# Kernel tuning notes

Hardware: AMD Instinct MI355X
Metric: run time of the kernel (lower is better)

## Reference

```python
import jax, jax.numpy as jnp
import numpy as np

F_DIM, H, O = 128, 256, 256
NQ, EQ = 64, 512
ND, ED = 50000, 600000

PARAM_SHAPES = [
    ("qW1", (F_DIM, H)), ("qb1", (H,)), ("qW2", (H, H)), ("qb2", (H,)),
    ("qW3", (H, H)),     ("qb3", (H,)), ("qW4", (H, O)), ("qb4", (O,)),
    ("dW1", (F_DIM, H)), ("db1", (H,)), ("dW2", (H, H)), ("db2", (H,)),
    ("dW3", (H, H)),     ("db3", (H,)), ("dW4", (H, O)), ("db4", (O,)),
    ("lW1", (2 * O, O)), ("lb1", (O,)),
    ("lW2", (O, O // 2)), ("lb2", (O // 2,)),
    ("lW3", (O // 2, 8)), ("lb3", (8,)),
]

def setup_inputs() -> dict:
    key = jax.random.key(0)
    ks = jax.random.split(key, 4 + len(PARAM_SHAPES))
    inp = {
        "query_in_feat": jax.random.normal(ks[0], (NQ, F_DIM), jnp.float32),
        "data_in_feat": jax.random.normal(ks[1], (ND, F_DIM), jnp.float32),
        "query_edge_list": jax.random.randint(ks[2], (2, EQ), 0, NQ),
        "data_edge_list": jax.random.randint(ks[3], (2, ED), 0, ND),
    }
    for i, (name, shape) in enumerate(PARAM_SHAPES):
        fan_in = shape[0] if len(shape) == 2 else 1
        inp[name] = jax.random.normal(ks[4 + i], shape, jnp.float32) * (1.0 / np.sqrt(fan_in))
    return inp

def _mlp2(x, W1, b1, W2, b2):
    return jnp.maximum(x @ W1 + b1, 0.0) @ W2 + b2

def _gin_conv(x, src, dst, W1, b1, W2, b2):
    # GINConv (eps=0): MLP(x_i + sum_{j->i} x_j); gather x[src], scatter-add at dst
    agg = jax.ops.segment_sum(x[src], dst, num_segments=x.shape[0])
    return _mlp2(x + agg, W1, b1, W2, b2)

def _gin(x, edge_index, p):
    src, dst = edge_index[0], edge_index[1]
    h = jnp.maximum(_gin_conv(x, src, dst, *p[:4]), 0.0)  # ReLU between convs
    return _gin_conv(h, src, dst, *p[4:])

def reference(query_in_feat, data_in_feat, query_edge_list, data_edge_list,
              qW1, qb1, qW2, qb2, qW3, qb3, qW4, qb4,
              dW1, db1, dW2, db2, dW3, db3, dW4, db4,
              lW1, lb1, lW2, lb2, lW3, lb3):
    qx = _gin(query_in_feat, query_edge_list, (qW1, qb1, qW2, qb2, qW3, qb3, qW4, qb4))
    dx = _gin(data_in_feat, data_edge_list, (dW1, db1, dW2, db2, dW3, db3, dW4, db4))
    # global_add_pool with batch = zeros -> single-graph sum
    qp = jnp.sum(qx, axis=0, keepdims=True)  # [1, O]
    dp = jnp.sum(dx, axis=0, keepdims=True)  # [1, O]
    h = jnp.concatenate([qp, dp], axis=1)    # [1, 2*O]
    h = jnp.maximum(h @ lW1 + lb1, 0.0)
    h = jnp.maximum(h @ lW2 + lb2, 0.0)
    h = jnp.maximum(h @ lW3 + lb3, 0.0)
    return h.reshape(1, 8)
```

## Files before the change

### kernel.cpp

```cpp
#include <hip/hip_runtime.h>
#include <hip/hip_bf16.h>


#define NQ 64
#define EQ 512
#define ND 50000
#define ED 600000
#define FDIM 128
#define HDIM 256

typedef __attribute__((ext_vector_type(8))) short short8;
typedef __attribute__((ext_vector_type(4))) float f32x4;
typedef __attribute__((ext_vector_type(2))) float floatx2;
typedef __attribute__((ext_vector_type(4))) unsigned short us4;
typedef __attribute__((ext_vector_type(2))) unsigned short us2;

__device__ __forceinline__ unsigned short f2bf(float f) {
    union { float f; unsigned u; } v; v.f = f;
    unsigned r = v.u + 0x7FFF + ((v.u >> 16) & 1);
    return (unsigned short)(r >> 16);
}
__device__ __forceinline__ float bf2f(unsigned short u) {
    union { unsigned u; float f; } v; v.u = ((unsigned)u) << 16;
    return v.f;
}


struct PackDesc {
    const float* W[8];
    unsigned short* Wp[8];
    int KT[8];
    int start[9];
};

__device__ __forceinline__ void pack_unit(const PackDesc& pd, int unit, int l) {
    int m = 0;
    while (m < 7 && unit >= pd.start[m + 1]) ++m;
    const int local = unit - pd.start[m];
    const int KT = pd.KT[m];
    const int kt = local % KT;
    const int ct = local / KT;
    const float* W = pd.W[m];
    unsigned short* Wp = pd.Wp[m];
    const int row = kt * 32 + (l >> 4) * 8;
    const int col = ct * 16 + (l & 15);
    short8 v;
#pragma unroll
    for (int j = 0; j < 8; ++j) v[j] = (short)f2bf(W[(size_t)(row + j) * 256 + col]);
    *(short8*)(Wp + (((size_t)(ct * KT + kt)) * 64 + l) * 8) = v;
}


__global__ void prepass(const float* __restrict__ xd, const float* __restrict__ xq,
                        unsigned short* __restrict__ bx, long long nd4, long long n4,
                        int cvt_b, PackDesc pd, int pack_units, int pack_b,
                        const int* __restrict__ d_dst, int* __restrict__ d_deg,
                        const int* __restrict__ q_dst, int* __restrict__ q_deg,
                        int d_eb) {
    const int b = blockIdx.x;
    const int tid = threadIdx.x;
    if (b < cvt_b) {
        long long i = (long long)b * 256 + tid;
        if (i >= n4) return;
        const float* src = (i < nd4) ? (xd + i * 4) : (xq + (i - nd4) * 4);
        float4 v = *(const float4*)src;
        us4 o;
        o[0] = f2bf(v.x); o[1] = f2bf(v.y); o[2] = f2bf(v.z); o[3] = f2bf(v.w);
        *(us4*)(bx + i * 4) = o;
    } else if (b < cvt_b + pack_b) {
        const int unit = (b - cvt_b) * 4 + (tid >> 6);
        if (unit < pack_units) pack_unit(pd, unit, tid & 63);
    } else {
        const int cb = b - cvt_b - pack_b;
        if (cb < d_eb) {
            int e = cb * 256 + tid;
            if (e < ED) atomicAdd(&d_deg[d_dst[e]], 1);
        } else {
            int e = (cb - d_eb) * 256 + tid;
            if (e < EQ) atomicAdd(&q_deg[q_dst[e]], 1);
        }
    }
}


__device__ __forceinline__ void scan1_body(const int* deg, int* rowptr, int* bsum,
                                           int n, int blk) {
    __shared__ int sh[256];
    const int t = threadIdx.x;
    const int i = blk * 256 + t;
    const int v = (i < n) ? deg[i] : 0;
    sh[t] = v;
    __syncthreads();
    for (int off = 1; off < 256; off <<= 1) {
        int x = (t >= off) ? sh[t - off] : 0;
        __syncthreads();
        sh[t] += x;
        __syncthreads();
    }
    if (i < n) rowptr[i] = sh[t] - v;
    if (t == 255) bsum[blk] = sh[255];
}

__global__ void scan_phase1_both(const int* __restrict__ d_deg, int* __restrict__ d_rowptr,
                                 int* __restrict__ d_bsum,
                                 const int* __restrict__ q_deg, int* __restrict__ q_rowptr,
                                 int* __restrict__ q_bsum, int dblocks) {
    int b = blockIdx.x;
    if (b < dblocks) scan1_body(d_deg, d_rowptr, d_bsum, ND, b);
    else             scan1_body(q_deg, q_rowptr, q_bsum, NQ, b - dblocks);
}

__device__ __forceinline__ void scan2_body(const int* bsum, int* boff, int* rowptr_n, int nb) {
    __shared__ int sh[256];
    const int t = threadIdx.x;
    const int v = (t < nb) ? bsum[t] : 0;
    sh[t] = v;
    __syncthreads();
    for (int off = 1; off < 256; off <<= 1) {
        int x = (t >= off) ? sh[t - off] : 0;
        __syncthreads();
        sh[t] += x;
        __syncthreads();
    }
    if (t < nb) boff[t] = sh[t] - v;
    if (t == 255) *rowptr_n = sh[255];
}

__global__ void scan_phase2_both(const int* __restrict__ d_bsum, int* __restrict__ d_boff,
                                 int* __restrict__ d_rowptr_n, int d_nb,
                                 const int* __restrict__ q_bsum, int* __restrict__ q_boff,
                                 int* __restrict__ q_rowptr_n, int q_nb) {
    if (blockIdx.x == 0) scan2_body(d_bsum, d_boff, d_rowptr_n, d_nb);
    else                 scan2_body(q_bsum, q_boff, q_rowptr_n, q_nb);
}

__global__ void scan_phase3_both(int* __restrict__ d_rowptr, const int* __restrict__ d_boff,
                                 int* __restrict__ d_cursor,
                                 int* __restrict__ q_rowptr, const int* __restrict__ q_boff,
                                 int* __restrict__ q_cursor, int dblocks) {
    int b = blockIdx.x;
    if (b < dblocks) {
        int i = b * 256 + threadIdx.x;
        if (i < ND) {
            int r = d_rowptr[i] + d_boff[b];
            d_rowptr[i] = r; d_cursor[i] = r;
        }
    } else {
        int i = (b - dblocks) * 256 + threadIdx.x;
        if (i < NQ) {
            int r = q_rowptr[i] + q_boff[b - dblocks];
            q_rowptr[i] = r; q_cursor[i] = r;
        }
    }
}

__global__ void fill_csr_both(const int* __restrict__ d_src, const int* __restrict__ d_dst,
                              int* __restrict__ d_cursor, int* __restrict__ d_csrsrc,
                              const int* __restrict__ q_src, const int* __restrict__ q_dst,
                              int* __restrict__ q_cursor, int* __restrict__ q_csrsrc,
                              int dblocks) {
    int b = blockIdx.x;
    if (b < dblocks) {
        int e = b * 256 + threadIdx.x;
        if (e < ED) {
            int p = atomicAdd(&d_cursor[d_dst[e]], 1);
            d_csrsrc[p] = d_src[e];
        }
    } else {
        int e = (b - dblocks) * 256 + threadIdx.x;
        if (e < EQ) {
            int p = atomicAdd(&q_cursor[q_dst[e]], 1);
            q_csrsrc[p] = q_src[e];
        }
    }
}


template <int F>
__global__ void gin_agg_dual(const unsigned short* __restrict__ xd, const int* __restrict__ rpd,
                             const int* __restrict__ csd, unsigned short* __restrict__ od,
                             const unsigned short* __restrict__ xq, const int* __restrict__ rpq,
                             const int* __restrict__ csq, unsigned short* __restrict__ oq) {
    constexpr int V = F / 64;
    const unsigned short* x; const int* rowptr; const int* csr; unsigned short* out; int node;
    if ((int)blockIdx.x < ND) { x = xd; rowptr = rpd; csr = csd; out = od; node = blockIdx.x; }
    else { x = xq; rowptr = rpq; csr = csq; out = oq; node = blockIdx.x - ND; }

    const int t = threadIdx.x;
    const int beg = rowptr[node];
    const int end = rowptr[node + 1];

    float acc[V];
    {
        const unsigned short* p = x + (size_t)node * F + t * V;
        if constexpr (V == 4) {
            us4 v = *(const us4*)p;
#pragma unroll
            for (int i = 0; i < 4; ++i) acc[i] = bf2f(v[i]);
        } else {
            us2 v = *(const us2*)p;
            acc[0] = bf2f(v[0]); acc[1] = bf2f(v[1]);
        }
    }
    int j = beg;
    for (; j + 1 < end; j += 2) {
        const unsigned short* p0 = x + (size_t)csr[j] * F + t * V;
        const unsigned short* p1 = x + (size_t)csr[j + 1] * F + t * V;
        if constexpr (V == 4) {
            us4 v0 = *(const us4*)p0;
            us4 v1 = *(const us4*)p1;
#pragma unroll
            for (int i = 0; i < 4; ++i) acc[i] += bf2f(v0[i]) + bf2f(v1[i]);
        } else {
            us2 v0 = *(const us2*)p0;
            us2 v1 = *(const us2*)p1;
            acc[0] += bf2f(v0[0]) + bf2f(v1[0]);
            acc[1] += bf2f(v0[1]) + bf2f(v1[1]);
        }
    }
    if (j < end) {
        const unsigned short* p0 = x + (size_t)csr[j] * F + t * V;
        if constexpr (V == 4) {
            us4 v0 = *(const us4*)p0;
#pragma unroll
            for (int i = 0; i < 4; ++i) acc[i] += bf2f(v0[i]);
        } else {
            us2 v0 = *(const us2*)p0;
            acc[0] += bf2f(v0[0]); acc[1] += bf2f(v0[1]);
        }
    }
    unsigned short* po = out + (size_t)node * F + t * V;
    if constexpr (V == 4) {
        us4 r;
#pragma unroll
        for (int i = 0; i < 4; ++i) r[i] = f2bf(acc[i]);
        *(us4*)po = r;
    } else {
        us2 r; r[0] = f2bf(acc[0]); r[1] = f2bf(acc[1]);
        *(us2*)po = r;
    }
}


__global__ void gin_agg_f8_dual(const unsigned char* __restrict__ xd, const int* __restrict__ rpd,
                                const int* __restrict__ csd, unsigned short* __restrict__ od,
                                const unsigned char* __restrict__ xq, const int* __restrict__ rpq,
                                const int* __restrict__ csq, unsigned short* __restrict__ oq) {
    const unsigned char* x; const int* rowptr; const int* csr; unsigned short* out; int node;
    if ((int)blockIdx.x < ND) { x = xd; rowptr = rpd; csr = csd; out = od; node = blockIdx.x; }
    else { x = xq; rowptr = rpq; csr = csq; out = oq; node = blockIdx.x - ND; }

    const int t = threadIdx.x;
    const int beg = rowptr[node];
    const int end = rowptr[node + 1];

    float a0, a1, a2, a3;
    {
        const unsigned w = *(const unsigned*)(x + (size_t)node * 256 + t * 4);
        floatx2 lo = __builtin_amdgcn_cvt_pk_f32_fp8((int)w, false);
        floatx2 hi = __builtin_amdgcn_cvt_pk_f32_fp8((int)w, true);
        a0 = lo[0]; a1 = lo[1]; a2 = hi[0]; a3 = hi[1];
    }
    int j = beg;
    for (; j + 1 < end; j += 2) {
        const unsigned w0 = *(const unsigned*)(x + (size_t)csr[j] * 256 + t * 4);
        const unsigned w1 = *(const unsigned*)(x + (size_t)csr[j + 1] * 256 + t * 4);
        floatx2 l0 = __builtin_amdgcn_cvt_pk_f32_fp8((int)w0, false);
        floatx2 h0 = __builtin_amdgcn_cvt_pk_f32_fp8((int)w0, true);
        floatx2 l1 = __builtin_amdgcn_cvt_pk_f32_fp8((int)w1, false);
        floatx2 h1 = __builtin_amdgcn_cvt_pk_f32_fp8((int)w1, true);
        a0 += l0[0] + l1[0]; a1 += l0[1] + l1[1];
        a2 += h0[0] + h1[0]; a3 += h0[1] + h1[1];
    }
    if (j < end) {
        const unsigned w0 = *(const unsigned*)(x + (size_t)csr[j] * 256 + t * 4);
        floatx2 l0 = __builtin_amdgcn_cvt_pk_f32_fp8((int)w0, false);
        floatx2 h0 = __builtin_amdgcn_cvt_pk_f32_fp8((int)w0, true);
        a0 += l0[0]; a1 += l0[1]; a2 += h0[0]; a3 += h0[1];
    }
    us4 r;
    r[0] = f2bf(a0); r[1] = f2bf(a1); r[2] = f2bf(a2); r[3] = f2bf(a3);
    *(us4*)(out + (size_t)node * 256 + t * 4) = r;
}


template <int KIN>
__global__ __launch_bounds__(256) void mlp_dual(
    const unsigned short* __restrict__ Ad,
    const unsigned short* __restrict__ W1pd, const float* __restrict__ b1d,
    const unsigned short* __restrict__ W2pd, const float* __restrict__ b2d,
    unsigned char* __restrict__ C8d, float* __restrict__ poold, int ndb,
    const unsigned short* __restrict__ Aq,
    const unsigned short* __restrict__ W1pq, const float* __restrict__ b1q,
    const unsigned short* __restrict__ W2pq, const float* __restrict__ b2q,
    unsigned char* __restrict__ C8q, float* __restrict__ poolq,
    int relu_out) {
    constexpr int KT1 = KIN / 32;
    __shared__ __align__(16) unsigned short lds[64 * 256];

    const unsigned short* A; const unsigned short* W1p; const float* b1;
    const unsigned short* W2p; const float* b2;
    unsigned char* C8; float* pool; int row0, N;
    if ((int)blockIdx.x < ndb) {
        A = Ad; W1p = W1pd; b1 = b1d; W2p = W2pd; b2 = b2d;
        C8 = C8d; pool = poold; row0 = blockIdx.x * 64; N = ND;
    } else {
        A = Aq; W1p = W1pq; b1 = b1q; W2p = W2pq; b2 = b2q;
        C8 = C8q; pool = poolq; row0 = 0; N = NQ;
    }

    const int tid = threadIdx.x;
    const int lane = tid & 63;
    const int wv = tid >> 6;
    const int lrow = lane & 15;
    const int lk2 = (lane >> 4) * 8;
    const int nrows = (N - row0 < 64) ? (N - row0) : 64;

    for (int idx = tid; idx < nrows * (KIN / 8); idx += 256) {
        const int r = idx / (KIN / 8);
        const int k8 = (idx % (KIN / 8)) * 8;
        short8 v = *(const short8*)(A + (size_t)(row0 + r) * KIN + k8);
        unsigned byte = (unsigned)((r * KIN + k8) * 2) ^ (unsigned)((r & 7) << 4);
        *(short8*)((char*)lds + byte) = v;
    }
    __syncthreads();

    f32x4 acc1[4][4];
#pragma unroll
    for (int fm = 0; fm < 4; ++fm)
#pragma unroll
        for (int fn = 0; fn < 4; ++fn) acc1[fm][fn] = (f32x4)(0.f);

    const unsigned short* W1Base = W1p + ((size_t)(wv * 4) * KT1 * 64 + lane) * 8;
    for (int kt = 0; kt < KT1; ++kt) {
        short8 a[4], bf[4];
#pragma unroll
        for (int fm = 0; fm < 4; ++fm) {
            const int r = fm * 16 + lrow;
            unsigned byte = (unsigned)((r * KIN + kt * 32 + lk2) * 2) ^ (unsigned)((r & 7) << 4);
            a[fm] = *(const short8*)((const char*)lds + byte);
        }
#pragma unroll
        for (int fn = 0; fn < 4; ++fn)
            bf[fn] = *(const short8*)(W1Base + ((size_t)fn * KT1 + kt) * 64 * 8);
#pragma unroll
        for (int fm = 0; fm < 4; ++fm)
#pragma unroll
            for (int fn = 0; fn < 4; ++fn)
                acc1[fm][fn] = __builtin_amdgcn_mfma_f32_16x16x32_bf16(
                    a[fm], bf[fn], acc1[fm][fn], 0, 0, 0);
    }
    __syncthreads();

#pragma unroll
    for (int fn = 0; fn < 4; ++fn) {
        const int col = wv * 64 + fn * 16 + lrow;
        const float bv = b1[col];
#pragma unroll
        for (int fm = 0; fm < 4; ++fm) {
            const int rbase = fm * 16 + (lane >> 4) * 4;
#pragma unroll
            for (int r = 0; r < 4; ++r) {
                const int row = rbase + r;
                const float v = fmaxf(acc1[fm][fn][r] + bv, 0.f);
                unsigned byte = (unsigned)((row * 256 + col) * 2) ^ (unsigned)((row & 7) << 4);
                *(unsigned short*)((char*)lds + byte) = f2bf(v);
            }
        }
    }
    __syncthreads();

    f32x4 acc2[4][4];
#pragma unroll
    for (int fm = 0; fm < 4; ++fm)
#pragma unroll
        for (int fn = 0; fn < 4; ++fn) acc2[fm][fn] = (f32x4)(0.f);

    const unsigned short* W2Base = W2p + ((size_t)(wv * 4) * 8 * 64 + lane) * 8;
    for (int kt = 0; kt < 8; ++kt) {
        short8 a[4], bf[4];
#pragma unroll
        for (int fm = 0; fm < 4; ++fm) {
            const int r = fm * 16 + lrow;
            unsigned byte = (unsigned)((r * 256 + kt * 32 + lk2) * 2) ^ (unsigned)((r & 7) << 4);
            a[fm] = *(const short8*)((const char*)lds + byte);
        }
#pragma unroll
        for (int fn = 0; fn < 4; ++fn)
            bf[fn] = *(const short8*)(W2Base + ((size_t)fn * 8 + kt) * 64 * 8);
#pragma unroll
        for (int fm = 0; fm < 4; ++fm)
#pragma unroll
            for (int fn = 0; fn < 4; ++fn)
                acc2[fm][fn] = __builtin_amdgcn_mfma_f32_16x16x32_bf16(
                    a[fm], bf[fn], acc2[fm][fn], 0, 0, 0);
    }

#pragma unroll
    for (int fn = 0; fn < 4; ++fn) {
        const int col = wv * 64 + fn * 16 + lrow;
        const float bv = b2[col];
        float ps = 0.f;
#pragma unroll
        for (int fm = 0; fm < 4; ++fm) {
            const int rbase = row0 + fm * 16 + (lane >> 4) * 4;
#pragma unroll
            for (int r = 0; r < 4; ++r) {
                const int row = rbase + r;
                if (row < N) {
                    float v = acc2[fm][fn][r] + bv;
                    if (relu_out) v = fmaxf(v, 0.f);
                    if (C8) {
                        unsigned p = (unsigned)__builtin_amdgcn_cvt_pk_fp8_f32(v, v, 0, false);
                        C8[(size_t)row * 256 + col] = (unsigned char)(p & 0xff);
                    }
                    ps += v;
                }
            }
        }
        if (pool) {
            ps += __shfl_xor(ps, 16);
            ps += __shfl_xor(ps, 32);
            if ((lane >> 4) == 0) atomicAdd(&pool[col], ps);
        }
    }
}


__global__ void mlp_head(const float* __restrict__ pooled,
                         const float* __restrict__ lW1, const float* __restrict__ lb1,
                         const float* __restrict__ lW2, const float* __restrict__ lb2,
                         const float* __restrict__ lW3, const float* __restrict__ lb3,
                         float* __restrict__ out) {
    __shared__ float h0[512];
    __shared__ float h1[256];
    __shared__ float h2[128];
    const int t = threadIdx.x;
    h0[t] = pooled[t];
    h0[t + 256] = pooled[t + 256];
    __syncthreads();

    float acc = lb1[t];
    for (int k = 0; k < 512; ++k) acc += h0[k] * lW1[k * 256 + t];
    h1[t] = fmaxf(acc, 0.f);
    __syncthreads();

    if (t < 128) {
        float a = lb2[t];
        for (int k = 0; k < 256; ++k) a += h1[k] * lW2[k * 128 + t];
        h2[t] = fmaxf(a, 0.f);
    }
    __syncthreads();

    if (t < 8) {
        float a = lb3[t];
        for (int k = 0; k < 128; ++k) a += h2[k] * lW3[k * 8 + t];
        out[t] = fmaxf(a, 0.f);
    }
}


extern "C" void kernel_launch(void* const* d_in, const int* in_sizes, int n_in,
                              void* d_out, int out_size, void* d_ws, size_t ws_size,
                              hipStream_t stream) {
    const float* q_x  = (const float*)d_in[0];
    const float* d_x  = (const float*)d_in[1];
    const int*   q_el = (const int*)d_in[2];
    const int*   d_el = (const int*)d_in[3];
    const float* qW1 = (const float*)d_in[4];  const float* qb1 = (const float*)d_in[5];
    const float* qW2 = (const float*)d_in[6];  const float* qb2 = (const float*)d_in[7];
    const float* qW3 = (const float*)d_in[8];  const float* qb3 = (const float*)d_in[9];
    const float* qW4 = (const float*)d_in[10]; const float* qb4 = (const float*)d_in[11];
    const float* dW1 = (const float*)d_in[12]; const float* db1 = (const float*)d_in[13];
    const float* dW2 = (const float*)d_in[14]; const float* db2 = (const float*)d_in[15];
    const float* dW3 = (const float*)d_in[16]; const float* db3 = (const float*)d_in[17];
    const float* dW4 = (const float*)d_in[18]; const float* db4 = (const float*)d_in[19];
    const float* lW1 = (const float*)d_in[20]; const float* lb1 = (const float*)d_in[21];
    const float* lW2 = (const float*)d_in[22]; const float* lb2 = (const float*)d_in[23];
    const float* lW3 = (const float*)d_in[24]; const float* lb3 = (const float*)d_in[25];
    (void)in_sizes; (void)n_in; (void)out_size; (void)ws_size;

    const int* q_src = q_el;  const int* q_dst = q_el + EQ;
    const int* d_src = d_el;  const int* d_dst = d_el + ED;

    char* wsb = (char*)d_ws;
    size_t off = 0;
    auto alloc = [&](size_t bytes) { void* p = wsb + off; off += (bytes + 255) & ~(size_t)255; return p; };

    unsigned short* bxd = (unsigned short*)alloc((size_t)ND * FDIM * 2);
    unsigned short* bxq = (unsigned short*)alloc((size_t)NQ * FDIM * 2);
    unsigned short* dag = (unsigned short*)alloc((size_t)ND * FDIM * 2);
    unsigned short* qag = (unsigned short*)alloc((size_t)NQ * FDIM * 2);
    unsigned char*  h8d = (unsigned char*)alloc((size_t)ND * HDIM);
    unsigned char*  h8q = (unsigned char*)alloc((size_t)NQ * HDIM);
    unsigned short* had = (unsigned short*)alloc((size_t)ND * HDIM * 2);
    unsigned short* haq = (unsigned short*)alloc((size_t)NQ * HDIM * 2);
    float* pooled = (float*)alloc(512 * 4);
    int* d_deg    = (int*)alloc((size_t)ND * 4);
    int* q_deg    = (int*)alloc((size_t)NQ * 4);
    int* d_rowptr = (int*)alloc((size_t)(ND + 1) * 4);
    int* d_cursor = (int*)alloc((size_t)ND * 4);
    int* d_csrsrc = (int*)alloc((size_t)ED * 4);
    int* d_bsum   = (int*)alloc(256 * 4);
    int* d_boff   = (int*)alloc(256 * 4);
    int* q_rowptr = (int*)alloc((size_t)(NQ + 1) * 4);
    int* q_cursor = (int*)alloc((size_t)NQ * 4);
    int* q_csrsrc = (int*)alloc((size_t)EQ * 4);
    int* q_bsum   = (int*)alloc(256 * 4);
    int* q_boff   = (int*)alloc(256 * 4);
    unsigned short* pdW1 = (unsigned short*)alloc((size_t)FDIM * 256 * 2);
    unsigned short* pdW2 = (unsigned short*)alloc((size_t)HDIM * 256 * 2);
    unsigned short* pdW3 = (unsigned short*)alloc((size_t)HDIM * 256 * 2);
    unsigned short* pdW4 = (unsigned short*)alloc((size_t)HDIM * 256 * 2);
    unsigned short* pqW1 = (unsigned short*)alloc((size_t)FDIM * 256 * 2);
    unsigned short* pqW2 = (unsigned short*)alloc((size_t)HDIM * 256 * 2);
    unsigned short* pqW3 = (unsigned short*)alloc((size_t)HDIM * 256 * 2);
    unsigned short* pqW4 = (unsigned short*)alloc((size_t)HDIM * 256 * 2);

    hipMemsetAsync(pooled, 0, 512 * 4, stream);
    hipMemsetAsync(d_deg, 0, (char*)(q_deg + NQ) - (char*)d_deg, stream);

    const int d_eb = (ED + 255) / 256;
    const int q_eb = (EQ + 255) / 256;
    const int d_nb = (ND + 255) / 256;
    const int q_nb = (NQ + 255) / 256;
    {
        PackDesc pd;
        const float* Ws[8] = {dW1, dW2, dW3, dW4, qW1, qW2, qW3, qW4};
        unsigned short* Wps[8] = {pdW1, pdW2, pdW3, pdW4, pqW1, pqW2, pqW3, pqW4};
        int kts[8] = {4, 8, 8, 8, 4, 8, 8, 8};
        int s = 0;
        for (int i = 0; i < 8; ++i) {
            pd.W[i] = Ws[i]; pd.Wp[i] = Wps[i]; pd.KT[i] = kts[i];
            pd.start[i] = s; s += 16 * kts[i];
        }
        pd.start[8] = s;
        const int pack_units = s;
        const int pack_b = (s + 3) / 4;
        long long nd4 = (long long)ND * FDIM / 4;
        long long n4 = nd4 + (long long)NQ * FDIM / 4;
        const int cvt_b = (int)((n4 + 255) / 256);
        prepass<<<cvt_b + pack_b + d_eb + q_eb, 256, 0, stream>>>(
            d_x, q_x, bxd, nd4, n4, cvt_b, pd, pack_units, pack_b,
            d_dst, d_deg, q_dst, q_deg, d_eb);
    }

    scan_phase1_both<<<d_nb + q_nb, 256, 0, stream>>>(d_deg, d_rowptr, d_bsum,
                                                      q_deg, q_rowptr, q_bsum, d_nb);
    scan_phase2_both<<<2, 256, 0, stream>>>(d_bsum, d_boff, d_rowptr + ND, d_nb,
                                            q_bsum, q_boff, q_rowptr + NQ, q_nb);
    scan_phase3_both<<<d_nb + q_nb, 256, 0, stream>>>(d_rowptr, d_boff, d_cursor,
                                                      q_rowptr, q_boff, q_cursor, d_nb);
    fill_csr_both<<<d_eb + q_eb, 256, 0, stream>>>(d_src, d_dst, d_cursor, d_csrsrc,
                                                   q_src, q_dst, q_cursor, q_csrsrc, d_eb);

    const int ndb = (ND + 63) / 64;

    gin_agg_dual<FDIM><<<ND + NQ, 64, 0, stream>>>(bxd, d_rowptr, d_csrsrc, dag,
                                                   bxq, q_rowptr, q_csrsrc, qag);
    mlp_dual<FDIM><<<ndb + 1, 256, 0, stream>>>(
        dag, pdW1, db1, pdW2, db2, h8d, nullptr, ndb,
        qag, pqW1, qb1, pqW2, qb2, h8q, nullptr, 1);

    gin_agg_f8_dual<<<ND + NQ, 64, 0, stream>>>(h8d, d_rowptr, d_csrsrc, had,
                                                h8q, q_rowptr, q_csrsrc, haq);
    mlp_dual<HDIM><<<ndb + 1, 256, 0, stream>>>(
        had, pdW3, db3, pdW4, db4, nullptr, pooled + 256, ndb,
        haq, pqW3, qb3, pqW4, qb4, nullptr, pooled, 0);

    mlp_head<<<1, 256, 0, stream>>>(pooled, lW1, lb1, lW2, lb2, lW3, lb3, (float*)d_out);
}
```

Measured before the change: 236.4 us.

## Store input features as FP8, pack two nodes per aggregation block, shrink MLP tiles

The input-feature conversion now writes FP8 instead of BF16, halving the bytes the first neighbour-gather kernel reads. The first aggregation kernel handles two nodes per 64-thread block, using 32 lanes per 128-wide row. The fused MLP kernels now process 32 rows per block instead of 64, doubling the block count and halving LDS and accumulator registers to raise occupancy. FP8 inputs lose precision relative to BF16. Note the query MLP launch passes the relu flag as 1 and 0 unchanged, and qmb is 2 blocks, which matches the new row0 indexing.

New measurement: 251.7 us. 1.06x slower.

```diff
diff --git a/kernel.cpp b/kernel.cpp
--- a/kernel.cpp
+++ b/kernel.cpp
@@ -52,7 +52,7 @@
 
 
 __global__ void prepass(const float* __restrict__ xd, const float* __restrict__ xq,
-                        unsigned short* __restrict__ bx, long long nd4, long long n4,
+                        unsigned char* __restrict__ x8, long long nd4, long long n4,
                         int cvt_b, PackDesc pd, int pack_units, int pack_b,
                         const int* __restrict__ d_dst, int* __restrict__ d_deg,
                         const int* __restrict__ q_dst, int* __restrict__ q_deg,
@@ -64,9 +64,9 @@
         if (i >= n4) return;
         const float* src = (i < nd4) ? (xd + i * 4) : (xq + (i - nd4) * 4);
         float4 v = *(const float4*)src;
-        us4 o;
-        o[0] = f2bf(v.x); o[1] = f2bf(v.y); o[2] = f2bf(v.z); o[3] = f2bf(v.w);
-        *(us4*)(bx + i * 4) = o;
+        int p = __builtin_amdgcn_cvt_pk_fp8_f32(v.x, v.y, 0, false);
+        p = __builtin_amdgcn_cvt_pk_fp8_f32(v.z, v.w, p, true);
+        *(unsigned*)(x8 + i * 4) = (unsigned)p;
     } else if (b < cvt_b + pack_b) {
         const int unit = (b - cvt_b) * 4 + (tid >> 6);
         if (unit < pack_units) pack_unit(pd, unit, tid & 63);
@@ -176,76 +176,48 @@
 }
 
 
-template <int F>
-__global__ void gin_agg_dual(const unsigned short* __restrict__ xd, const int* __restrict__ rpd,
-                             const int* __restrict__ csd, unsigned short* __restrict__ od,
-                             const unsigned short* __restrict__ xq, const int* __restrict__ rpq,
-                             const int* __restrict__ csq, unsigned short* __restrict__ oq) {
-    constexpr int V = F / 64;
-    const unsigned short* x; const int* rowptr; const int* csr; unsigned short* out; int node;
-    if ((int)blockIdx.x < ND) { x = xd; rowptr = rpd; csr = csd; out = od; node = blockIdx.x; }
-    else { x = xq; rowptr = rpq; csr = csq; out = oq; node = blockIdx.x - ND; }
+__global__ void gin_agg_f8_128_dual(const unsigned char* __restrict__ xd,
+                                    const int* __restrict__ rpd, const int* __restrict__ csd,
+                                    unsigned short* __restrict__ od,
+                                    const unsigned char* __restrict__ xq,
+                                    const int* __restrict__ rpq, const int* __restrict__ csq,
+                                    unsigned short* __restrict__ oq, int ndpair) {
+    const unsigned char* x; const int* rowptr; const int* csr; unsigned short* out; int nb;
+    if ((int)blockIdx.x < ndpair) { x = xd; rowptr = rpd; csr = csd; out = od; nb = blockIdx.x; }
+    else { x = xq; rowptr = rpq; csr = csq; out = oq; nb = blockIdx.x - ndpair; }
 
     const int t = threadIdx.x;
+    const int node = nb * 2 + (t >> 5);
+    const int c = t & 31;
+
     const int beg = rowptr[node];
     const int end = rowptr[node + 1];
 
-    float acc[V];
+    float a0, a1, a2, a3;
     {
-        const unsigned short* p = x + (size_t)node * F + t * V;
-        if constexpr (V == 4) {
-            us4 v = *(const us4*)p;
-#pragma unroll
-            for (int i = 0; i < 4; ++i) acc[i] = bf2f(v[i]);
-        } else {
-            us2 v = *(const us2*)p;
-            acc[0] = bf2f(v[0]); acc[1] = bf2f(v[1]);
-        }
-    }
-    int j = beg;
-    for (; j + 1 < end; j += 2) {
-        const unsigned short* p0 = x + (size_t)csr[j] * F + t * V;
-        const unsigned short* p1 = x + (size_t)csr[j + 1] * F + t * V;
-        if constexpr (V == 4) {
-            us4 v0 = *(const us4*)p0;
-            us4 v1 = *(const us4*)p1;
-#pragma unroll
-            for (int i = 0; i < 4; ++i) acc[i] += bf2f(v0[i]) + bf2f(v1[i]);
-        } else {
-            us2 v0 = *(const us2*)p0;
-            us2 v1 = *(const us2*)p1;
-            acc[0] += bf2f(v0[0]) + bf2f(v1[0]);
-            acc[1] += bf2f(v0[1]) + bf2f(v1[1]);
-        }
-    }
-    if (j < end) {
-        const unsigned short* p0 = x + (size_t)csr[j] * F + t * V;
-        if constexpr (V == 4) {
-            us4 v0 = *(const us4*)p0;
-#pragma unroll
-            for (int i = 0; i < 4; ++i) acc[i] += bf2f(v0[i]);
-        } else {
-            us2 v0 = *(const us2*)p0;
-            acc[0] += bf2f(v0[0]); acc[1] += bf2f(v0[1]);
-        }
-    }
-    unsigned short* po = out + (size_t)node * F + t * V;
-    if constexpr (V == 4) {
-        us4 r;
-#pragma unroll
-        for (int i = 0; i < 4; ++i) r[i] = f2bf(acc[i]);
-        *(us4*)po = r;
-    } else {
-        us2 r; r[0] = f2bf(acc[0]); r[1] = f2bf(acc[1]);
-        *(us2*)po = r;
-    }
-}
-
-
-__global__ void gin_agg_f8_dual(const unsigned char* __restrict__ xd, const int* __restrict__ rpd,
-                                const int* __restrict__ csd, unsigned short* __restrict__ od,
-                                const unsigned char* __restrict__ xq, const int* __restrict__ rpq,
-                                const int* __restrict__ csq, unsigned short* __restrict__ oq) {
+        const unsigned w = *(const unsigned*)(x + (size_t)node * 128 + c * 4);
+        floatx2 lo = __builtin_amdgcn_cvt_pk_f32_fp8((int)w, false);
+        floatx2 hi = __builtin_amdgcn_cvt_pk_f32_fp8((int)w, true);
+        a0 = lo[0]; a1 = lo[1]; a2 = hi[0]; a3 = hi[1];
+    }
+    for (int j = beg; j < end; ++j) {
+        const unsigned w = *(const unsigned*)(x + (size_t)csr[j] * 128 + c * 4);
+        floatx2 lo = __builtin_amdgcn_cvt_pk_f32_fp8((int)w, false);
+        floatx2 hi = __builtin_amdgcn_cvt_pk_f32_fp8((int)w, true);
+        a0 += lo[0]; a1 += lo[1]; a2 += hi[0]; a3 += hi[1];
+    }
+    us4 r;
+    r[0] = f2bf(a0); r[1] = f2bf(a1); r[2] = f2bf(a2); r[3] = f2bf(a3);
+    *(us4*)(out + (size_t)node * 128 + c * 4) = r;
+}
+
+
+__global__ void gin_agg_f8_256_dual(const unsigned char* __restrict__ xd,
+                                    const int* __restrict__ rpd, const int* __restrict__ csd,
+                                    unsigned short* __restrict__ od,
+                                    const unsigned char* __restrict__ xq,
+                                    const int* __restrict__ rpq, const int* __restrict__ csq,
+                                    unsigned short* __restrict__ oq) {
     const unsigned char* x; const int* rowptr; const int* csr; unsigned short* out; int node;
     if ((int)blockIdx.x < ND) { x = xd; rowptr = rpd; csr = csd; out = od; node = blockIdx.x; }
     else { x = xq; rowptr = rpq; csr = csq; out = oq; node = blockIdx.x - ND; }
@@ -289,24 +261,24 @@
     const unsigned short* __restrict__ Ad,
     const unsigned short* __restrict__ W1pd, const float* __restrict__ b1d,
     const unsigned short* __restrict__ W2pd, const float* __restrict__ b2d,
-    unsigned char* __restrict__ C8d, float* __restrict__ poold, int ndb,
+    unsigned char* __restrict__ C8d, float* __restrict__ poold, int nmb,
     const unsigned short* __restrict__ Aq,
     const unsigned short* __restrict__ W1pq, const float* __restrict__ b1q,
     const unsigned short* __restrict__ W2pq, const float* __restrict__ b2q,
     unsigned char* __restrict__ C8q, float* __restrict__ poolq,
     int relu_out) {
     constexpr int KT1 = KIN / 32;
-    __shared__ __align__(16) unsigned short lds[64 * 256];
+    __shared__ __align__(16) unsigned short lds[32 * 256];
 
     const unsigned short* A; const unsigned short* W1p; const float* b1;
     const unsigned short* W2p; const float* b2;
     unsigned char* C8; float* pool; int row0, N;
-    if ((int)blockIdx.x < ndb) {
+    if ((int)blockIdx.x < nmb) {
         A = Ad; W1p = W1pd; b1 = b1d; W2p = W2pd; b2 = b2d;
-        C8 = C8d; pool = poold; row0 = blockIdx.x * 64; N = ND;
+        C8 = C8d; pool = poold; row0 = blockIdx.x * 32; N = ND;
     } else {
         A = Aq; W1p = W1pq; b1 = b1q; W2p = W2pq; b2 = b2q;
-        C8 = C8q; pool = poolq; row0 = 0; N = NQ;
+        C8 = C8q; pool = poolq; row0 = (blockIdx.x - nmb) * 32; N = NQ;
     }
 
     const int tid = threadIdx.x;
@@ -314,7 +286,7 @@
     const int wv = tid >> 6;
     const int lrow = lane & 15;
     const int lk2 = (lane >> 4) * 8;
-    const int nrows = (N - row0 < 64) ? (N - row0) : 64;
+    const int nrows = (N - row0 < 32) ? (N - row0) : 32;
 
     for (int idx = tid; idx < nrows * (KIN / 8); idx += 256) {
         const int r = idx / (KIN / 8);
@@ -325,17 +297,17 @@
     }
     __syncthreads();
 
-    f32x4 acc1[4][4];
-#pragma unroll
-    for (int fm = 0; fm < 4; ++fm)
+    f32x4 acc1[2][4];
+#pragma unroll
+    for (int fm = 0; fm < 2; ++fm)
 #pragma unroll
         for (int fn = 0; fn < 4; ++fn) acc1[fm][fn] = (f32x4)(0.f);
 
     const unsigned short* W1Base = W1p + ((size_t)(wv * 4) * KT1 * 64 + lane) * 8;
     for (int kt = 0; kt < KT1; ++kt) {
-        short8 a[4], bf[4];
-#pragma unroll
-        for (int fm = 0; fm < 4; ++fm) {
+        short8 a[2], bf[4];
+#pragma unroll
+        for (int fm = 0; fm < 2; ++fm) {
             const int r = fm * 16 + lrow;
             unsigned byte = (unsigned)((r * KIN + kt * 32 + lk2) * 2) ^ (unsigned)((r & 7) << 4);
             a[fm] = *(const short8*)((const char*)lds + byte);
@@ -344,7 +316,7 @@
         for (int fn = 0; fn < 4; ++fn)
             bf[fn] = *(const short8*)(W1Base + ((size_t)fn * KT1 + kt) * 64 * 8);
 #pragma unroll
-        for (int fm = 0; fm < 4; ++fm)
+        for (int fm = 0; fm < 2; ++fm)
 #pragma unroll
             for (int fn = 0; fn < 4; ++fn)
                 acc1[fm][fn] = __builtin_amdgcn_mfma_f32_16x16x32_bf16(
@@ -357,7 +329,7 @@
         const int col = wv * 64 + fn * 16 + lrow;
         const float bv = b1[col];
 #pragma unroll
-        for (int fm = 0; fm < 4; ++fm) {
+        for (int fm = 0; fm < 2; ++fm) {
             const int rbase = fm * 16 + (lane >> 4) * 4;
 #pragma unroll
             for (int r = 0; r < 4; ++r) {
@@ -370,17 +342,17 @@
     }
     __syncthreads();
 
-    f32x4 acc2[4][4];
-#pragma unroll
-    for (int fm = 0; fm < 4; ++fm)
+    f32x4 acc2[2][4];
+#pragma unroll
+    for (int fm = 0; fm < 2; ++fm)
 #pragma unroll
         for (int fn = 0; fn < 4; ++fn) acc2[fm][fn] = (f32x4)(0.f);
 
     const unsigned short* W2Base = W2p + ((size_t)(wv * 4) * 8 * 64 + lane) * 8;
     for (int kt = 0; kt < 8; ++kt) {
-        short8 a[4], bf[4];
-#pragma unroll
-        for (int fm = 0; fm < 4; ++fm) {
+        short8 a[2], bf[4];
+#pragma unroll
+        for (int fm = 0; fm < 2; ++fm) {
             const int r = fm * 16 + lrow;
             unsigned byte = (unsigned)((r * 256 + kt * 32 + lk2) * 2) ^ (unsigned)((r & 7) << 4);
             a[fm] = *(const short8*)((const char*)lds + byte);
@@ -389,7 +361,7 @@
         for (int fn = 0; fn < 4; ++fn)
             bf[fn] = *(const short8*)(W2Base + ((size_t)fn * 8 + kt) * 64 * 8);
 #pragma unroll
-        for (int fm = 0; fm < 4; ++fm)
+        for (int fm = 0; fm < 2; ++fm)
 #pragma unroll
             for (int fn = 0; fn < 4; ++fn)
                 acc2[fm][fn] = __builtin_amdgcn_mfma_f32_16x16x32_bf16(
@@ -402,7 +374,7 @@
         const float bv = b2[col];
         float ps = 0.f;
 #pragma unroll
-        for (int fm = 0; fm < 4; ++fm) {
+        for (int fm = 0; fm < 2; ++fm) {
             const int rbase = row0 + fm * 16 + (lane >> 4) * 4;
 #pragma unroll
             for (int r = 0; r < 4; ++r) {
@@ -487,8 +459,8 @@
     size_t off = 0;
     auto alloc = [&](size_t bytes) { void* p = wsb + off; off += (bytes + 255) & ~(size_t)255; return p; };
 
-    unsigned short* bxd = (unsigned short*)alloc((size_t)ND * FDIM * 2);
-    unsigned short* bxq = (unsigned short*)alloc((size_t)NQ * FDIM * 2);
+    unsigned char*  x8d = (unsigned char*)alloc((size_t)ND * FDIM);
+    unsigned char*  x8q = (unsigned char*)alloc((size_t)NQ * FDIM);
     unsigned short* dag = (unsigned short*)alloc((size_t)ND * FDIM * 2);
     unsigned short* qag = (unsigned short*)alloc((size_t)NQ * FDIM * 2);
     unsigned char*  h8d = (unsigned char*)alloc((size_t)ND * HDIM);
@@ -541,7 +513,7 @@
         long long n4 = nd4 + (long long)NQ * FDIM / 4;
         const int cvt_b = (int)((n4 + 255) / 256);
         prepass<<<cvt_b + pack_b + d_eb + q_eb, 256, 0, stream>>>(
-            d_x, q_x, bxd, nd4, n4, cvt_b, pd, pack_units, pack_b,
+            d_x, q_x, x8d, nd4, n4, cvt_b, pd, pack_units, pack_b,
             d_dst, d_deg, q_dst, q_deg, d_eb);
     }
 
@@ -554,18 +526,21 @@
     fill_csr_both<<<d_eb + q_eb, 256, 0, stream>>>(d_src, d_dst, d_cursor, d_csrsrc,
                                                    q_src, q_dst, q_cursor, q_csrsrc, d_eb);
 
-    const int ndb = (ND + 63) / 64;
-
-    gin_agg_dual<FDIM><<<ND + NQ, 64, 0, stream>>>(bxd, d_rowptr, d_csrsrc, dag,
-                                                   bxq, q_rowptr, q_csrsrc, qag);
-    mlp_dual<FDIM><<<ndb + 1, 256, 0, stream>>>(
-        dag, pdW1, db1, pdW2, db2, h8d, nullptr, ndb,
+    const int ndpair = ND / 2;
+    const int qpair = NQ / 2;
+    const int nmb = (ND + 31) / 32;
+    const int qmb = (NQ + 31) / 32;
+
+    gin_agg_f8_128_dual<<<ndpair + qpair, 64, 0, stream>>>(
+        x8d, d_rowptr, d_csrsrc, dag, x8q, q_rowptr, q_csrsrc, qag, ndpair);
+    mlp_dual<FDIM><<<nmb + qmb, 256, 0, stream>>>(
+        dag, pdW1, db1, pdW2, db2, h8d, nullptr, nmb,
         qag, pqW1, qb1, pqW2, qb2, h8q, nullptr, 1);
 
-    gin_agg_f8_dual<<<ND + NQ, 64, 0, stream>>>(h8d, d_rowptr, d_csrsrc, had,
-                                                h8q, q_rowptr, q_csrsrc, haq);
-    mlp_dual<HDIM><<<ndb + 1, 256, 0, stream>>>(
-        had, pdW3, db3, pdW4, db4, nullptr, pooled + 256, ndb,
+    gin_agg_f8_256_dual<<<ND + NQ, 64, 0, stream>>>(
+        h8d, d_rowptr, d_csrsrc, had, h8q, q_rowptr, q_csrsrc, haq);
+    mlp_dual<HDIM><<<nmb + qmb, 256, 0, stream>>>(
+        had, pdW3, db3, pdW4, db4, nullptr, pooled + 256, nmb,
         haq, pqW3, qb3, pqW4, qb4, nullptr, pooled, 0);
 
     mlp_head<<<1, 256, 0, stream>>>(pooled, lW1, lb1, lW2, lb2, lW3, lb3, (float*)d_out);
```

## Pool before final linear layer, fold W4 into head kernel

Applied to the files above, without the earlier changes.

Because the last GIN linear layer has no output ReLU, the sum-pool commutes with it. The second MLP now pools relu(x@W3+b3) directly, and the head applies W4 plus N*b4 to the pooled vector. This removes the per-node 256x256 GEMM, the LDS staging of the hidden layer, and W4 packing. The new t1pool kernel reads A straight from global memory without LDS, and the query buffer is padded so the unmasked row loads stay in bounds.

Measured after the change: 245.0 us. 1.04x slower.

```diff
diff --git a/kernel.cpp b/kernel.cpp
--- a/kernel.cpp
+++ b/kernel.cpp
@@ -242,10 +242,12 @@
 }
 
 
-__global__ void gin_agg_f8_dual(const unsigned char* __restrict__ xd, const int* __restrict__ rpd,
-                                const int* __restrict__ csd, unsigned short* __restrict__ od,
-                                const unsigned char* __restrict__ xq, const int* __restrict__ rpq,
-                                const int* __restrict__ csq, unsigned short* __restrict__ oq) {
+__global__ void gin_agg_f8_256_dual(const unsigned char* __restrict__ xd,
+                                    const int* __restrict__ rpd, const int* __restrict__ csd,
+                                    unsigned short* __restrict__ od,
+                                    const unsigned char* __restrict__ xq,
+                                    const int* __restrict__ rpq, const int* __restrict__ csq,
+                                    unsigned short* __restrict__ oq) {
     const unsigned char* x; const int* rowptr; const int* csr; unsigned short* out; int node;
     if ((int)blockIdx.x < ND) { x = xd; rowptr = rpd; csr = csd; out = od; node = blockIdx.x; }
     else { x = xq; rowptr = rpq; csr = csq; out = oq; node = blockIdx.x - ND; }
@@ -289,24 +291,23 @@
     const unsigned short* __restrict__ Ad,
     const unsigned short* __restrict__ W1pd, const float* __restrict__ b1d,
     const unsigned short* __restrict__ W2pd, const float* __restrict__ b2d,
-    unsigned char* __restrict__ C8d, float* __restrict__ poold, int ndb,
+    unsigned char* __restrict__ C8d, int ndb,
     const unsigned short* __restrict__ Aq,
     const unsigned short* __restrict__ W1pq, const float* __restrict__ b1q,
     const unsigned short* __restrict__ W2pq, const float* __restrict__ b2q,
-    unsigned char* __restrict__ C8q, float* __restrict__ poolq,
-    int relu_out) {
+    unsigned char* __restrict__ C8q) {
     constexpr int KT1 = KIN / 32;
     __shared__ __align__(16) unsigned short lds[64 * 256];
 
     const unsigned short* A; const unsigned short* W1p; const float* b1;
     const unsigned short* W2p; const float* b2;
-    unsigned char* C8; float* pool; int row0, N;
+    unsigned char* C8; int row0, N;
     if ((int)blockIdx.x < ndb) {
         A = Ad; W1p = W1pd; b1 = b1d; W2p = W2pd; b2 = b2d;
-        C8 = C8d; pool = poold; row0 = blockIdx.x * 64; N = ND;
+        C8 = C8d; row0 = blockIdx.x * 64; N = ND;
     } else {
         A = Aq; W1p = W1pq; b1 = b1q; W2p = W2pq; b2 = b2q;
-        C8 = C8q; pool = poolq; row0 = 0; N = NQ;
+        C8 = C8q; row0 = 0; N = NQ;
     }
 
     const int tid = threadIdx.x;
@@ -400,7 +401,6 @@
     for (int fn = 0; fn < 4; ++fn) {
         const int col = wv * 64 + fn * 16 + lrow;
         const float bv = b2[col];
-        float ps = 0.f;
 #pragma unroll
         for (int fm = 0; fm < 4; ++fm) {
             const int rbase = row0 + fm * 16 + (lane >> 4) * 4;
@@ -408,26 +408,87 @@
             for (int r = 0; r < 4; ++r) {
                 const int row = rbase + r;
                 if (row < N) {
-                    float v = acc2[fm][fn][r] + bv;
-                    if (relu_out) v = fmaxf(v, 0.f);
-                    if (C8) {
-                        unsigned p = (unsigned)__builtin_amdgcn_cvt_pk_fp8_f32(v, v, 0, false);
-                        C8[(size_t)row * 256 + col] = (unsigned char)(p & 0xff);
-                    }
-                    ps += v;
+                    float v = fmaxf(acc2[fm][fn][r] + bv, 0.f);
+                    unsigned p = (unsigned)__builtin_amdgcn_cvt_pk_fp8_f32(v, v, 0, false);
+                    C8[(size_t)row * 256 + col] = (unsigned char)(p & 0xff);
                 }
             }
         }
-        if (pool) {
-            ps += __shfl_xor(ps, 16);
-            ps += __shfl_xor(ps, 32);
-            if ((lane >> 4) == 0) atomicAdd(&pool[col], ps);
-        }
-    }
-}
-
-
-__global__ void mlp_head(const float* __restrict__ pooled,
+    }
+}
+
+
+__global__ __launch_bounds__(256) void t1pool_dual(
+    const unsigned short* __restrict__ Ad,
+    const unsigned short* __restrict__ W1pd, const float* __restrict__ b1d,
+    float* __restrict__ poold, int ndb,
+    const unsigned short* __restrict__ Aq,
+    const unsigned short* __restrict__ W1pq, const float* __restrict__ b1q,
+    float* __restrict__ poolq) {
+    const unsigned short* A; const unsigned short* W1p; const float* b1;
+    float* pool; int row0, N;
+    if ((int)blockIdx.x < ndb) {
+        A = Ad; W1p = W1pd; b1 = b1d; pool = poold; row0 = blockIdx.x * 64; N = ND;
+    } else {
+        A = Aq; W1p = W1pq; b1 = b1q; pool = poolq; row0 = 0; N = NQ;
+    }
+
+    const int tid = threadIdx.x;
+    const int lane = tid & 63;
+    const int wv = tid >> 6;
+    const int lrow = lane & 15;
+    const int lk2 = (lane >> 4) * 8;
+
+    f32x4 acc[4][4];
+#pragma unroll
+    for (int fm = 0; fm < 4; ++fm)
+#pragma unroll
+        for (int fn = 0; fn < 4; ++fn) acc[fm][fn] = (f32x4)(0.f);
+
+    const unsigned short* W1Base = W1p + ((size_t)(wv * 4) * 8 * 64 + lane) * 8;
+    const unsigned short* Alane = A + (size_t)(row0 + lrow) * 256 + lk2;
+
+#pragma unroll
+    for (int kt = 0; kt < 8; ++kt) {
+        short8 a[4], bf[4];
+#pragma unroll
+        for (int fm = 0; fm < 4; ++fm)
+            a[fm] = *(const short8*)(Alane + (size_t)(fm * 16) * 256 + kt * 32);
+#pragma unroll
+        for (int fn = 0; fn < 4; ++fn)
+            bf[fn] = *(const short8*)(W1Base + ((size_t)fn * 8 + kt) * 64 * 8);
+#pragma unroll
+        for (int fm = 0; fm < 4; ++fm)
+#pragma unroll
+            for (int fn = 0; fn < 4; ++fn)
+                acc[fm][fn] = __builtin_amdgcn_mfma_f32_16x16x32_bf16(
+                    a[fm], bf[fn], acc[fm][fn], 0, 0, 0);
+    }
+
+#pragma unroll
+    for (int fn = 0; fn < 4; ++fn) {
+        const int col = wv * 64 + fn * 16 + lrow;
+        const float bv = b1[col];
+        float ps = 0.f;
+#pragma unroll
+        for (int fm = 0; fm < 4; ++fm) {
+            const int rbase = row0 + fm * 16 + (lane >> 4) * 4;
+#pragma unroll
+            for (int r = 0; r < 4; ++r) {
+                const int row = rbase + r;
+                if (row < N) ps += fmaxf(acc[fm][fn][r] + bv, 0.f);
+            }
+        }
+        ps += __shfl_xor(ps, 16);
+        ps += __shfl_xor(ps, 32);
+        if ((lane >> 4) == 0) atomicAdd(&pool[col], ps);
+    }
+}
+
+
+__global__ void mlp_head(const float* __restrict__ poolT1,
+                         const float* __restrict__ qW4, const float* __restrict__ qb4,
+                         const float* __restrict__ dW4, const float* __restrict__ db4,
                          const float* __restrict__ lW1, const float* __restrict__ lb1,
                          const float* __restrict__ lW2, const float* __restrict__ lb2,
                          const float* __restrict__ lW3, const float* __restrict__ lb3,
@@ -436,8 +497,15 @@
     __shared__ float h1[256];
     __shared__ float h2[128];
     const int t = threadIdx.x;
-    h0[t] = pooled[t];
-    h0[t + 256] = pooled[t + 256];
+
+    float accq = (float)NQ * qb4[t];
+    float accd = (float)ND * db4[t];
+    for (int k = 0; k < 256; ++k) {
+        accq += poolT1[k] * qW4[(size_t)k * 256 + t];
+        accd += poolT1[256 + k] * dW4[(size_t)k * 256 + t];
+    }
+    h0[t] = accq;
+    h0[t + 256] = accd;
     __syncthreads();
 
     float acc = lb1[t];
@@ -494,8 +562,8 @@
     unsigned char*  h8d = (unsigned char*)alloc((size_t)ND * HDIM);
     unsigned char*  h8q = (unsigned char*)alloc((size_t)NQ * HDIM);
     unsigned short* had = (unsigned short*)alloc((size_t)ND * HDIM * 2);
-    unsigned short* haq = (unsigned short*)alloc((size_t)NQ * HDIM * 2);
-    float* pooled = (float*)alloc(512 * 4);
+    unsigned short* haq = (unsigned short*)alloc((size_t)(NQ + 64) * HDIM * 2);
+    float* poolT1 = (float*)alloc(512 * 4);
     int* d_deg    = (int*)alloc((size_t)ND * 4);
     int* q_deg    = (int*)alloc((size_t)NQ * 4);
     int* d_rowptr = (int*)alloc((size_t)(ND + 1) * 4);
@@ -511,13 +579,11 @@
     unsigned short* pdW1 = (unsigned short*)alloc((size_t)FDIM * 256 * 2);
     unsigned short* pdW2 = (unsigned short*)alloc((size_t)HDIM * 256 * 2);
     unsigned short* pdW3 = (unsigned short*)alloc((size_t)HDIM * 256 * 2);
-    unsigned short* pdW4 = (unsigned short*)alloc((size_t)HDIM * 256 * 2);
     unsigned short* pqW1 = (unsigned short*)alloc((size_t)FDIM * 256 * 2);
     unsigned short* pqW2 = (unsigned short*)alloc((size_t)HDIM * 256 * 2);
     unsigned short* pqW3 = (unsigned short*)alloc((size_t)HDIM * 256 * 2);
-    unsigned short* pqW4 = (unsigned short*)alloc((size_t)HDIM * 256 * 2);
-
-    hipMemsetAsync(pooled, 0, 512 * 4, stream);
+
+    hipMemsetAsync(poolT1, 0, 512 * 4, stream);
     hipMemsetAsync(d_deg, 0, (char*)(q_deg + NQ) - (char*)d_deg, stream);
 
     const int d_eb = (ED + 255) / 256;
@@ -526,14 +592,15 @@
     const int q_nb = (NQ + 255) / 256;
     {
         PackDesc pd;
-        const float* Ws[8] = {dW1, dW2, dW3, dW4, qW1, qW2, qW3, qW4};
-        unsigned short* Wps[8] = {pdW1, pdW2, pdW3, pdW4, pqW1, pqW2, pqW3, pqW4};
-        int kts[8] = {4, 8, 8, 8, 4, 8, 8, 8};
+        const float* Ws[6] = {dW1, dW2, dW3, qW1, qW2, qW3};
+        unsigned short* Wps[6] = {pdW1, pdW2, pdW3, pqW1, pqW2, pqW3};
+        int kts[6] = {4, 8, 8, 4, 8, 8};
         int s = 0;
-        for (int i = 0; i < 8; ++i) {
+        for (int i = 0; i < 6; ++i) {
             pd.W[i] = Ws[i]; pd.Wp[i] = Wps[i]; pd.KT[i] = kts[i];
             pd.start[i] = s; s += 16 * kts[i];
         }
+        for (int i = 6; i < 8; ++i) { pd.W[i] = dW1; pd.Wp[i] = pdW1; pd.KT[i] = 4; pd.start[i] = s; }
         pd.start[8] = s;
         const int pack_units = s;
         const int pack_b = (s + 3) / 4;
@@ -559,14 +626,15 @@
     gin_agg_dual<FDIM><<<ND + NQ, 64, 0, stream>>>(bxd, d_rowptr, d_csrsrc, dag,
                                                    bxq, q_rowptr, q_csrsrc, qag);
     mlp_dual<FDIM><<<ndb + 1, 256, 0, stream>>>(
-        dag, pdW1, db1, pdW2, db2, h8d, nullptr, ndb,
-        qag, pqW1, qb1, pqW2, qb2, h8q, nullptr, 1);
-
-    gin_agg_f8_dual<<<ND + NQ, 64, 0, stream>>>(h8d, d_rowptr, d_csrsrc, had,
-                                                h8q, q_rowptr, q_csrsrc, haq);
-    mlp_dual<HDIM><<<ndb + 1, 256, 0, stream>>>(
-        had, pdW3, db3, pdW4, db4, nullptr, pooled + 256, ndb,
-        haq, pqW3, qb3, pqW4, qb4, nullptr, pooled, 0);
-
-    mlp_head<<<1, 256, 0, stream>>>(pooled, lW1, lb1, lW2, lb2, lW3, lb3, (float*)d_out);
-}
+        dag, pdW1, db1, pdW2, db2, h8d, ndb,
+        qag, pqW1, qb1, pqW2, qb2, h8q);
+
+    gin_agg_f8_256_dual<<<ND + NQ, 64, 0, stream>>>(
+        h8d, d_rowptr, d_csrsrc, had, h8q, q_rowptr, q_csrsrc, haq);
+    t1pool_dual<<<ndb + 1, 256, 0, stream>>>(
+        had, pdW3, db3, poolT1 + 256, ndb,
+        haq, pqW3, qb3, poolT1);
+
+    mlp_head<<<1, 256, 0, stream>>>(poolT1, qW4, qb4, dW4, db4,
+                                    lW1, lb1, lW2, lb2, lW3, lb3, (float*)d_out);
+}
```
